# Kernel optimization log

Measured on AMD Instinct MI355X. Metric: run time of the kernel, lower is better.

Reference implementation:

```python
import jax, jax.numpy as jnp
import numpy as np

BETA = 1.0
POWER_ITERS = 9
EPS = 1e-12  # F.normalize default eps


def _normalize(v):
    # L2 normalize over dim=1 of [B, N, 1], matching F.normalize(x, dim=1)
    n = jnp.linalg.norm(v, axis=1, keepdims=True)
    return v / jnp.maximum(n, EPS)


def _dominant_eigenvalue(A, x):
    # A: [B, N, N], x: [B, N, 1]
    for _ in range(POWER_ITERS):
        x = _normalize(jnp.matmul(A, x))
    Ax = jnp.matmul(A, x)[..., 0]              # [B, N]
    num = jnp.sum(Ax * x[..., 0], axis=1)      # x^T A x
    den = jnp.sum(x[..., 0] ** 2, axis=1)      # ||x||^2 (== 1 after normalize)
    return num / den, x


def setup_inputs() -> dict:
    key = jax.random.key(0)
    k1, k2 = jax.random.split(key)
    B, C, H, W = 256, 2048, 7, 7
    x = jax.random.normal(k1, (B, C, H, W), dtype=jnp.float32)
    x0 = _normalize(jax.random.normal(k2, (B, H * W, 1), dtype=jnp.float32))
    return {"x": x, "x0": x0}


def reference(x, x0):
    B, C, H, W = x.shape
    N = H * W
    Wm = x.reshape(B, C, N)
    # ATA = W^T W : [B, N, N]
    ATA = jnp.einsum('bcn,bcm->bnm', Wm, Wm)
    # first power iteration: largest eigenvalue; x0 is a no_grad constant
    largest, x1 = _dominant_eigenvalue(ATA, jax.lax.stop_gradient(x0))
    I = jnp.eye(N, dtype=ATA.dtype)
    shifted = ATA - largest[:, None, None] * I
    # second power iteration warm-started from detached x1 (torch stores last_x detached)
    tmp, _ = _dominant_eigenvalue(shifted, jax.lax.stop_gradient(x1))
    smallest = tmp + largest
    penalty = BETA * (largest / smallest - 1.0) ** 2
    return jnp.sum(penalty) / B
```

## Files before the change

### kernel.cpp

```cpp
#include <hip/hip_runtime.h>
#include <hip/hip_bf16.h>
#include <stdint.h>


#define BATCH 256
#define CDIM  2048
#define NDIM  49
#define GROUPS 4
#define GK    (CDIM / GROUPS)
#define CHUNK 64
#define NCHUNK (GK / CHUNK)
#define ITEMS (NDIM * (CHUNK / 8))
#define CHUNK_FLOATS (CHUNK * NDIM)

typedef __bf16 bf16x8 __attribute__((ext_vector_type(8)));
typedef float  f32x16 __attribute__((ext_vector_type(16)));
typedef float  f32x4  __attribute__((ext_vector_type(4)));

union V16 {
  f32x4  f4;
  bf16x8 b8;
};

__device__ __forceinline__ void load8(const float* __restrict__ g,
                                      float (&r)[8]) {
#pragma unroll
  for (int j = 0; j < 8; ++j) r[j] = g[j * NDIM];
}

__device__ __forceinline__ void cvt_store(const float (&r)[8], float* Hb,
                                          float* Lb, int w) {
  bf16x8 hv, lv;
#pragma unroll
  for (int j = 0; j < 8; ++j) {
    float e = r[j];
    __bf16 h = (__bf16)e;
    hv[j] = h;
    lv[j] = (__bf16)(e - (float)h);
  }
  V16 a, b;
  a.b8 = hv;
  b.b8 = lv;
  *(f32x4*)(Hb + w) = a.f4;
  *(f32x4*)(Lb + w) = b.f4;
}

__device__ __forceinline__ void comp16(const float* Hb, const float* Lb,
                                       int m, int n, int hf, f32x16& c1,
                                       f32x16& c2, f32x16& c3) {
  const f32x4* H = (const f32x4*)Hb;
  const f32x4* L = (const f32x4*)Lb;
#pragma unroll
  for (int s = 0; s < 4; ++s) {
    const int blk = 2 * s + hf;
    V16 ah, al, bh, bl;
    ah.f4 = H[m * 8 + (blk ^ (m & 7))];
    al.f4 = L[m * 8 + (blk ^ (m & 7))];
    bh.f4 = H[n * 8 + (blk ^ (n & 7))];
    bl.f4 = L[n * 8 + (blk ^ (n & 7))];
    c1 = __builtin_amdgcn_mfma_f32_32x32x16_bf16(ah.b8, bh.b8, c1, 0, 0, 0);
    c2 = __builtin_amdgcn_mfma_f32_32x32x16_bf16(ah.b8, bl.b8, c2, 0, 0, 0);
    c3 = __builtin_amdgcn_mfma_f32_32x32x16_bf16(al.b8, bh.b8, c3, 0, 0, 0);
  }
}

__global__ __launch_bounds__(1024) void fused_kernel(
    const float* __restrict__ x, const float* __restrict__ x0,
    float* __restrict__ pen) {
  __shared__ __align__(16) float lds[32768];

  const int tid  = threadIdx.x;
  const int b    = blockIdx.x;
  const int g    = tid >> 8;
  const int ltid = tid & 255;
  const int lane = tid & 63;
  const int gw   = (tid >> 6) & 3;
  const int ln   = lane & 31;
  const int hf   = lane >> 5;
  const int qm = gw >> 1, qn = gw & 1;
  const int m = qm * 32 + ln;
  const int n = qn * 32 + ln;

  float* const buf0 = lds + g * 8192;
  float* const buf1 = lds + g * 8192 + 4096;

  const float* gbase = x + (size_t)b * (CDIM * NDIM)
                         + (size_t)g * (GK * NDIM);

  const int i0 = ltid;
  const int i1 = ltid + 256;
  const bool v1 = (i1 < ITEMS);
  const int kq0 = (i0 * 1338) >> 16;
  const int n0  = i0 - 49 * kq0;
  const int kq1 = (i1 * 1338) >> 16;
  const int n1  = i1 - 49 * kq1;
  const int g0  = kq0 * (8 * NDIM) + n0;
  const int g1  = kq1 * (8 * NDIM) + n1;
  const int w0  = n0 * 32 + 4 * (kq0 ^ (n0 & 7));
  const int w1  = n1 * 32 + 4 * (kq1 ^ (n1 & 7));

  f32x16 c1, c2, c3;
#pragma unroll
  for (int i = 0; i < 16; ++i) { c1[i] = 0.f; c2[i] = 0.f; c3[i] = 0.f; }

  float sA0[8], sA1[8], sB0[8], sB1[8];

  load8(gbase + g0, sA0);
  if (v1) load8(gbase + g1, sA1);

#pragma unroll
  for (int ch = 0; ch < NCHUNK; ch += 2) {
    {
      const float* gch = gbase + (size_t)(ch + 1) * CHUNK_FLOATS;
      load8(gch + g0, sB0);
      if (v1) load8(gch + g1, sB1);
    }
    cvt_store(sA0, buf0, buf0 + 2048, w0);
    if (v1) cvt_store(sA1, buf0, buf0 + 2048, w1);
    __syncthreads();
    comp16(buf0, buf0 + 2048, m, n, hf, c1, c2, c3);

    if (ch + 2 < NCHUNK) {
      const float* gch = gbase + (size_t)(ch + 2) * CHUNK_FLOATS;
      load8(gch + g0, sA0);
      if (v1) load8(gch + g1, sA1);
    }
    cvt_store(sB0, buf1, buf1 + 2048, w0);
    if (v1) cvt_store(sB1, buf1, buf1 + 2048, w1);
    __syncthreads();
    comp16(buf1, buf1 + 2048, m, n, hf, c1, c2, c3);
  }

  float* A = lds;
  __syncthreads();
#pragma unroll
  for (int gg = 0; gg < GROUPS; ++gg) {
    if (g == gg) {
#pragma unroll
      for (int r = 0; r < 16; ++r) {
        int row = (r & 3) + 8 * (r >> 2) + 4 * hf;
        int mm = qm * 32 + row;
        if (mm < NDIM && n < NDIM) {
          float v = c1[r] + c2[r] + c3[r];
          if (gg == 0) A[mm * NDIM + n] = v;
          else         A[mm * NDIM + n] += v;
        }
      }
    }
    __syncthreads();
  }

  if (tid < 64) {
    const bool act = (tid < NDIM);
    float Ar[NDIM];
    {
      const float* Arow = &A[(act ? tid : (NDIM - 1)) * NDIM];
#pragma unroll
      for (int k = 0; k < NDIM; ++k) Ar[k] = Arow[k];
    }
    float xl = act ? x0[b * NDIM + tid] : 0.f;

    auto rayleigh = [&](float shift) -> float {
      for (int it = 0; it < 9; ++it) {
        float a0 = 0.f, a1 = 0.f, a2 = 0.f, a3 = 0.f;
#pragma unroll
        for (int k = 0; k < 48; k += 4) {
          a0 = fmaf(Ar[k + 0], __shfl(xl, k + 0, 64), a0);
          a1 = fmaf(Ar[k + 1], __shfl(xl, k + 1, 64), a1);
          a2 = fmaf(Ar[k + 2], __shfl(xl, k + 2, 64), a2);
          a3 = fmaf(Ar[k + 3], __shfl(xl, k + 3, 64), a3);
        }
        a0 = fmaf(Ar[48], __shfl(xl, 48, 64), a0);
        float y = act ? (((a0 + a1) + (a2 + a3)) - shift * xl) : 0.f;
        float s2 = y * y;
#pragma unroll
        for (int o = 32; o; o >>= 1) s2 += __shfl_xor(s2, o, 64);
        xl = y / fmaxf(sqrtf(s2), 1e-12f);
      }
      float a0 = 0.f, a1 = 0.f, a2 = 0.f, a3 = 0.f;
#pragma unroll
      for (int k = 0; k < 48; k += 4) {
        a0 = fmaf(Ar[k + 0], __shfl(xl, k + 0, 64), a0);
        a1 = fmaf(Ar[k + 1], __shfl(xl, k + 1, 64), a1);
        a2 = fmaf(Ar[k + 2], __shfl(xl, k + 2, 64), a2);
        a3 = fmaf(Ar[k + 3], __shfl(xl, k + 3, 64), a3);
      }
      a0 = fmaf(Ar[48], __shfl(xl, 48, 64), a0);
      float yy = act ? (((a0 + a1) + (a2 + a3)) - shift * xl) : 0.f;
      float num = yy * xl;
      float den = xl * xl;
#pragma unroll
      for (int o = 32; o; o >>= 1) {
        num += __shfl_xor(num, o, 64);
        den += __shfl_xor(den, o, 64);
      }
      return num / den;
    };

    float largest  = rayleigh(0.f);
    float smallest = rayleigh(largest) + largest;
    if (tid == 0) {
      float r = largest / smallest - 1.f;
      pen[b] = r * r;
    }
  }
}

__global__ __launch_bounds__(64) void finish_kernel(
    const float* __restrict__ pen, float* __restrict__ out) {
  const int t = threadIdx.x;
  float s = pen[t] + pen[t + 64] + pen[t + 128] + pen[t + 192];
#pragma unroll
  for (int o = 32; o; o >>= 1) s += __shfl_xor(s, o, 64);
  if (t == 0) out[0] = s * (1.0f / (float)BATCH);
}

extern "C" void kernel_launch(void* const* d_in, const int* in_sizes, int n_in,
                              void* d_out, int out_size, void* d_ws,
                              size_t ws_size, hipStream_t stream) {
  const float* x  = (const float*)d_in[0];
  const float* x0 = (const float*)d_in[1];
  float* out = (float*)d_out;
  float* pen = (float*)d_ws;

  fused_kernel<<<BATCH, 1024, 0, stream>>>(x, x0, pen);
  finish_kernel<<<1, 64, 0, stream>>>(pen, out);
}
```

Measured before the change: 168.3 us.

## Load MFMA operands directly from global into registers, bypassing LDS staging

Replaces the cooperative global→LDS staging (split into bf16 hi/lo with a swizzled layout, guarded by barriers) with per-lane direct global loads of the MFMA operand fragments. The bf16 split happens in registers and the loads are double-buffered across 16-channel slices. Diagonal-quadrant waves reuse their A fragment as B and skip the second load. This removes the LDS round trip and the per-chunk __syncthreads, at the cost of redundant global reads across waves, uncoalesced strided per-lane loads, and clamped duplicate reads for rows past 49.

```diff
diff --git a/kernel.cpp b/kernel.cpp
--- a/kernel.cpp
+++ b/kernel.cpp
@@ -7,131 +7,79 @@
 #define CDIM  2048
 #define NDIM  49
 #define GROUPS 4
-#define GK    (CDIM / GROUPS)
-#define CHUNK 64
-#define NCHUNK (GK / CHUNK)
-#define ITEMS (NDIM * (CHUNK / 8))
-#define CHUNK_FLOATS (CHUNK * NDIM)
+#define GK     (CDIM / GROUPS)
+#define NSLICE (GK / 16)
+#define SLICE_FLOATS (16 * NDIM)
 
 typedef __bf16 bf16x8 __attribute__((ext_vector_type(8)));
 typedef float  f32x16 __attribute__((ext_vector_type(16)));
-typedef float  f32x4  __attribute__((ext_vector_type(4)));
-
-union V16 {
-  f32x4  f4;
-  bf16x8 b8;
-};
-
-__device__ __forceinline__ void load8(const float* __restrict__ g,
-                                      float (&r)[8]) {
-#pragma unroll
-  for (int j = 0; j < 8; ++j) r[j] = g[j * NDIM];
-}
-
-__device__ __forceinline__ void cvt_store(const float (&r)[8], float* Hb,
-                                          float* Lb, int w) {
-  bf16x8 hv, lv;
-#pragma unroll
-  for (int j = 0; j < 8; ++j) {
-    float e = r[j];
-    __bf16 h = (__bf16)e;
-    hv[j] = h;
-    lv[j] = (__bf16)(e - (float)h);
-  }
-  V16 a, b;
-  a.b8 = hv;
-  b.b8 = lv;
-  *(f32x4*)(Hb + w) = a.f4;
-  *(f32x4*)(Lb + w) = b.f4;
-}
-
-__device__ __forceinline__ void comp16(const float* Hb, const float* Lb,
-                                       int m, int n, int hf, f32x16& c1,
-                                       f32x16& c2, f32x16& c3) {
-  const f32x4* H = (const f32x4*)Hb;
-  const f32x4* L = (const f32x4*)Lb;
-#pragma unroll
-  for (int s = 0; s < 4; ++s) {
-    const int blk = 2 * s + hf;
-    V16 ah, al, bh, bl;
-    ah.f4 = H[m * 8 + (blk ^ (m & 7))];
-    al.f4 = L[m * 8 + (blk ^ (m & 7))];
-    bh.f4 = H[n * 8 + (blk ^ (n & 7))];
-    bl.f4 = L[n * 8 + (blk ^ (n & 7))];
-    c1 = __builtin_amdgcn_mfma_f32_32x32x16_bf16(ah.b8, bh.b8, c1, 0, 0, 0);
-    c2 = __builtin_amdgcn_mfma_f32_32x32x16_bf16(ah.b8, bl.b8, c2, 0, 0, 0);
-    c3 = __builtin_amdgcn_mfma_f32_32x32x16_bf16(al.b8, bh.b8, c3, 0, 0, 0);
-  }
-}
 
 __global__ __launch_bounds__(1024) void fused_kernel(
     const float* __restrict__ x, const float* __restrict__ x0,
     float* __restrict__ pen) {
-  __shared__ __align__(16) float lds[32768];
+  __shared__ __align__(16) float A[NDIM * NDIM + 3];
 
   const int tid  = threadIdx.x;
   const int b    = blockIdx.x;
   const int g    = tid >> 8;
-  const int ltid = tid & 255;
   const int lane = tid & 63;
   const int gw   = (tid >> 6) & 3;
-  const int ln   = lane & 31;
+  const int l5   = lane & 31;
   const int hf   = lane >> 5;
   const int qm = gw >> 1, qn = gw & 1;
-  const int m = qm * 32 + ln;
-  const int n = qn * 32 + ln;
-
-  float* const buf0 = lds + g * 8192;
-  float* const buf1 = lds + g * 8192 + 4096;
+  const int m = qm * 32 + l5;
+  const int n = qn * 32 + l5;
+  const int ca = (m < NDIM) ? m : (NDIM - 1);
+  const int cb = (n < NDIM) ? n : (NDIM - 1);
+  const int offA = hf * (8 * NDIM) + ca;
+  const int offB = hf * (8 * NDIM) + cb;
+  const bool same = (qm == qn);
 
   const float* gbase = x + (size_t)b * (CDIM * NDIM)
                          + (size_t)g * (GK * NDIM);
-
-  const int i0 = ltid;
-  const int i1 = ltid + 256;
-  const bool v1 = (i1 < ITEMS);
-  const int kq0 = (i0 * 1338) >> 16;
-  const int n0  = i0 - 49 * kq0;
-  const int kq1 = (i1 * 1338) >> 16;
-  const int n1  = i1 - 49 * kq1;
-  const int g0  = kq0 * (8 * NDIM) + n0;
-  const int g1  = kq1 * (8 * NDIM) + n1;
-  const int w0  = n0 * 32 + 4 * (kq0 ^ (n0 & 7));
-  const int w1  = n1 * 32 + 4 * (kq1 ^ (n1 & 7));
 
   f32x16 c1, c2, c3;
 #pragma unroll
   for (int i = 0; i < 16; ++i) { c1[i] = 0.f; c2[i] = 0.f; c3[i] = 0.f; }
 
-  float sA0[8], sA1[8], sB0[8], sB1[8];
+  float a0[8], b0[8], a1[8], b1[8];
 
-  load8(gbase + g0, sA0);
-  if (v1) load8(gbase + g1, sA1);
+  auto LOAD = [&](int s, float (&a)[8], float (&bb)[8]) {
+    const float* p = gbase + s * SLICE_FLOATS;
+#pragma unroll
+    for (int j = 0; j < 8; ++j) a[j] = p[j * NDIM + offA];
+    if (!same) {
+#pragma unroll
+      for (int j = 0; j < 8; ++j) bb[j] = p[j * NDIM + offB];
+    }
+  };
+  auto CVT = [&](const float (&r)[8], bf16x8& hi, bf16x8& lo) {
+#pragma unroll
+    for (int j = 0; j < 8; ++j) {
+      float e = r[j];
+      __bf16 h = (__bf16)e;
+      hi[j] = h;
+      lo[j] = (__bf16)(e - (float)h);
+    }
+  };
+  auto COMPUTE = [&](const float (&a)[8], const float (&bb)[8]) {
+    bf16x8 ah, al, bh, bl;
+    CVT(a, ah, al);
+    if (same) { bh = ah; bl = al; }
+    else      CVT(bb, bh, bl);
+    c1 = __builtin_amdgcn_mfma_f32_32x32x16_bf16(ah, bh, c1, 0, 0, 0);
+    c2 = __builtin_amdgcn_mfma_f32_32x32x16_bf16(ah, bl, c2, 0, 0, 0);
+    c3 = __builtin_amdgcn_mfma_f32_32x32x16_bf16(al, bh, c3, 0, 0, 0);
+  };
 
-#pragma unroll
-  for (int ch = 0; ch < NCHUNK; ch += 2) {
-    {
-      const float* gch = gbase + (size_t)(ch + 1) * CHUNK_FLOATS;
-      load8(gch + g0, sB0);
-      if (v1) load8(gch + g1, sB1);
-    }
-    cvt_store(sA0, buf0, buf0 + 2048, w0);
-    if (v1) cvt_store(sA1, buf0, buf0 + 2048, w1);
-    __syncthreads();
-    comp16(buf0, buf0 + 2048, m, n, hf, c1, c2, c3);
-
-    if (ch + 2 < NCHUNK) {
-      const float* gch = gbase + (size_t)(ch + 2) * CHUNK_FLOATS;
-      load8(gch + g0, sA0);
-      if (v1) load8(gch + g1, sA1);
-    }
-    cvt_store(sB0, buf1, buf1 + 2048, w0);
-    if (v1) cvt_store(sB1, buf1, buf1 + 2048, w1);
-    __syncthreads();
-    comp16(buf1, buf1 + 2048, m, n, hf, c1, c2, c3);
+  LOAD(0, a0, b0);
+  for (int s = 0; s < NSLICE; s += 2) {
+    LOAD(s + 1, a1, b1);
+    COMPUTE(a0, b0);
+    if (s + 2 < NSLICE) LOAD(s + 2, a0, b0);
+    COMPUTE(a1, b1);
   }
 
-  float* A = lds;
   __syncthreads();
 #pragma unroll
   for (int gg = 0; gg < GROUPS; ++gg) {
@@ -162,31 +110,31 @@
 
     auto rayleigh = [&](float shift) -> float {
       for (int it = 0; it < 9; ++it) {
-        float a0 = 0.f, a1 = 0.f, a2 = 0.f, a3 = 0.f;
+        float a0r = 0.f, a1r = 0.f, a2r = 0.f, a3r = 0.f;
 #pragma unroll
         for (int k = 0; k < 48; k += 4) {
-          a0 = fmaf(Ar[k + 0], __shfl(xl, k + 0, 64), a0);
-          a1 = fmaf(Ar[k + 1], __shfl(xl, k + 1, 64), a1);
-          a2 = fmaf(Ar[k + 2], __shfl(xl, k + 2, 64), a2);
-          a3 = fmaf(Ar[k + 3], __shfl(xl, k + 3, 64), a3);
+          a0r = fmaf(Ar[k + 0], __shfl(xl, k + 0, 64), a0r);
+          a1r = fmaf(Ar[k + 1], __shfl(xl, k + 1, 64), a1r);
+          a2r = fmaf(Ar[k + 2], __shfl(xl, k + 2, 64), a2r);
+          a3r = fmaf(Ar[k + 3], __shfl(xl, k + 3, 64), a3r);
         }
-        a0 = fmaf(Ar[48], __shfl(xl, 48, 64), a0);
-        float y = act ? (((a0 + a1) + (a2 + a3)) - shift * xl) : 0.f;
+        a0r = fmaf(Ar[48], __shfl(xl, 48, 64), a0r);
+        float y = act ? (((a0r + a1r) + (a2r + a3r)) - shift * xl) : 0.f;
         float s2 = y * y;
 #pragma unroll
         for (int o = 32; o; o >>= 1) s2 += __shfl_xor(s2, o, 64);
         xl = y / fmaxf(sqrtf(s2), 1e-12f);
       }
-      float a0 = 0.f, a1 = 0.f, a2 = 0.f, a3 = 0.f;
+      float a0r = 0.f, a1r = 0.f, a2r = 0.f, a3r = 0.f;
 #pragma unroll
       for (int k = 0; k < 48; k += 4) {
-        a0 = fmaf(Ar[k + 0], __shfl(xl, k + 0, 64), a0);
-        a1 = fmaf(Ar[k + 1], __shfl(xl, k + 1, 64), a1);
-        a2 = fmaf(Ar[k + 2], __shfl(xl, k + 2, 64), a2);
-        a3 = fmaf(Ar[k + 3], __shfl(xl, k + 3, 64), a3);
+        a0r = fmaf(Ar[k + 0], __shfl(xl, k + 0, 64), a0r);
+        a1r = fmaf(Ar[k + 1], __shfl(xl, k + 1, 64), a1r);
+        a2r = fmaf(Ar[k + 2], __shfl(xl, k + 2, 64), a2r);
+        a3r = fmaf(Ar[k + 3], __shfl(xl, k + 3, 64), a3r);
       }
-      a0 = fmaf(Ar[48], __shfl(xl, 48, 64), a0);
-      float yy = act ? (((a0 + a1) + (a2 + a3)) - shift * xl) : 0.f;
+      a0r = fmaf(Ar[48], __shfl(xl, 48, 64), a0r);
+      float yy = act ? (((a0r + a1r) + (a2r + a3r)) - shift * xl) : 0.f;
       float num = yy * xl;
       float den = xl * xl;
 #pragma unroll
```

New measurement: 175.3 us. 1.04x slower.
